# Kernel optimization log

Measured on AMD Instinct MI355X. Metric: run time of the kernel, lower is better.

The kernel has to match this reference:

```python
import jax, jax.numpy as jnp
import numpy as np

N = 100_000   # nodes
D = 64        # hidden = H * C
H, C = 8, 8   # heads, per-head channels
E = 500_000   # edges per edge set
EPS = 1e-3    # keras LayerNormalization default epsilon
RSQRT_C = np.float32(1.0 / np.sqrt(C))


def setup_inputs() -> dict:
    key = jax.random.key(0)
    ks = jax.random.split(key, 13)
    s = 0.05
    return dict(
        x=jax.random.normal(ks[0], (N, D), jnp.float32),
        src0=jax.random.randint(ks[1], (E,), 0, N, jnp.int32),
        dst0=jax.random.randint(ks[2], (E,), 0, N, jnp.int32),
        src1=jax.random.randint(ks[3], (E,), 0, N, jnp.int32),
        dst1=jax.random.randint(ks[4], (E,), 0, N, jnp.int32),
        Wk=jax.random.normal(ks[5], (D, D), jnp.float32) * s,
        bk=jnp.zeros((D,), jnp.float32),
        Wm=jax.random.normal(ks[6], (D, D), jnp.float32) * s,
        bm=jnp.zeros((D,), jnp.float32),
        Wq=jax.random.normal(ks[7], (D, D), jnp.float32) * s,
        bq=jnp.zeros((D,), jnp.float32),
        Wa=jax.random.normal(ks[8], (D, D), jnp.float32) * s,
        ba=jnp.zeros((D,), jnp.float32),
        Watt0=jax.random.normal(ks[9], (H, C, C), jnp.float32) * s,
        Wmsg0=jax.random.normal(ks[10], (H, C, C), jnp.float32) * s,
        prior0=jnp.ones((H,), jnp.float32),
        Watt1=jax.random.normal(ks[11], (H, C, C), jnp.float32) * s,
        Wmsg1=jax.random.normal(ks[12], (H, C, C), jnp.float32) * s,
        prior1=jnp.ones((H,), jnp.float32),
        skip_w=jnp.ones((1,), jnp.float32),
        ln_gamma=jnp.ones((D,), jnp.float32),
        ln_beta=jnp.zeros((D,), jnp.float32),
    )


def _edge_terms(k, m, q, src, dst, Watt, Wmsg, prior):
    # gather sender keys/messages, apply per-edge-set per-head projections
    ke = jnp.einsum('ehk,hkl->ehl', k[src], Watt)          # [E,H,C]
    score = jnp.einsum('ehc,ehc->eh', ke, q[dst]) * prior * RSQRT_C  # [E,H]
    me = jnp.einsum('ehk,hkl->ehl', m[src], Wmsg)          # [E,H,C]
    return score, me


def _forward(x, src0, dst0, src1, dst1, Wk, bk, Wm, bm, Wq, bq, Wa, ba,
             Watt0, Wmsg0, prior0, Watt1, Wmsg1, prior1,
             skip_w, ln_gamma, ln_beta):
    n = x.shape[0]
    split = lambda t: t.reshape(n, H, C)
    k = split(x @ Wk + bk)   # sender keys   [N,H,C]
    m = split(x @ Wm + bm)   # sender msgs   [N,H,C]
    q = split(x @ Wq + bq)   # receiver qrys [N,H,C]

    s0, m0 = _edge_terms(k, m, q, src0, dst0, Watt0, Wmsg0, prior0)
    s1, m1 = _edge_terms(k, m, q, src1, dst1, Watt1, Wmsg1, prior1)

    # joint segment softmax over ALL incoming edges per receiver (across edge sets)
    scores = jnp.concatenate([s0, s1], axis=0)  # [Et,H]
    msgs = jnp.concatenate([m0, m1], axis=0)    # [Et,H,C]
    recv = jnp.concatenate([dst0, dst1], axis=0)
    smax = jax.ops.segment_max(scores, recv, num_segments=n)
    ex = jnp.exp(scores - smax[recv])
    denom = jax.ops.segment_sum(ex, recv, num_segments=n)
    coef = ex / denom[recv]                      # [Et,H]

    pooled = jax.ops.segment_sum(coef[:, :, None] * msgs, recv, num_segments=n)  # [N,H,C]
    merged = pooled.reshape(n, D)
    agg = jax.nn.gelu(merged, approximate=False) @ Wa + ba
    # (dropout_rate=0.0 -> identity)
    sc = jax.nn.sigmoid(skip_w[0])               # learnable weighted skip
    out = sc * agg + (1.0 - sc) * x
    # layer norm (keras default eps=1e-3)
    mu = jnp.mean(out, axis=-1, keepdims=True)
    var = jnp.var(out, axis=-1, keepdims=True)
    return ln_gamma * (out - mu) * jax.lax.rsqrt(var + EPS) + ln_beta


def reference(x, src0, dst0, src1, dst1, Wk, bk, Wm, bm, Wq, bq, Wa, ba,
              Watt0, Wmsg0, prior0, Watt1, Wmsg1, prior1,
              skip_w, ln_gamma, ln_beta):
    return _forward(x, src0, dst0, src1, dst1, Wk, bk, Wm, bm, Wq, bq, Wa, ba,
                    Watt0, Wmsg0, prior0, Watt1, Wmsg1, prior1,
                    skip_w, ln_gamma, ln_beta)
```

## Files before the change

### kernel.cpp

```cpp
#include <hip/hip_runtime.h>
#include <cstdint>
#include <cstddef>

#define TPB 256
static constexpr float RSQRT_C_F = 0.35355339059327373f;

typedef __attribute__((ext_vector_type(8))) short bf16x8;
typedef __attribute__((ext_vector_type(4))) float f32x4;

__device__ __forceinline__ unsigned short f2bf(float f) {
    unsigned u = __float_as_uint(f);
    u += 0x7FFFu + ((u >> 16) & 1u);
    return (unsigned short)(u >> 16);
}
__device__ __forceinline__ float bf2f(unsigned short h) {
    return __uint_as_float((unsigned)h << 16);
}

__global__ void prep1_kernel(const float* __restrict__ Wq, const float* __restrict__ bq,
                             const float* __restrict__ Wk, const float* __restrict__ bk,
                             const float* __restrict__ Wm, const float* __restrict__ bm,
                             const float* __restrict__ Watt0, const float* __restrict__ prior0,
                             const float* __restrict__ Watt1, const float* __restrict__ prior1,
                             const float* __restrict__ Wmsg0, const float* __restrict__ Wmsg1,
                             float* __restrict__ Wbig, float* __restrict__ bbig) {
    int idx = blockIdx.x * TPB + threadIdx.x;
    if (idx < 64 * 320) {
        int i = idx / 320, col = idx % 320;
        float v;
        if (col < 64) {
            v = Wq[i * 64 + col];
        } else {
            int j = col - 64, set = j >> 6, l = j & 63, h = l >> 3, lc = l & 7;
            const float* Win = (set < 2) ? Wk : Wm;
            const float* T = (set == 0) ? Watt0 : (set == 1) ? Watt1 : (set == 2) ? Wmsg0 : Wmsg1;
            float scale = (set == 0) ? prior0[h] * RSQRT_C_F
                        : (set == 1) ? prior1[h] * RSQRT_C_F : 1.f;
            float acc = 0.f;
            #pragma unroll
            for (int c = 0; c < 8; c++) acc += Win[i * 64 + h * 8 + c] * T[h * 64 + c * 8 + lc];
            v = acc * scale;
        }
        Wbig[idx] = v;
    } else if (idx < 64 * 320 + 320) {
        int col = idx - 64 * 320;
        float v;
        if (col < 64) {
            v = bq[col];
        } else {
            int j = col - 64, set = j >> 6, l = j & 63, h = l >> 3, lc = l & 7;
            const float* bin = (set < 2) ? bk : bm;
            const float* T = (set == 0) ? Watt0 : (set == 1) ? Watt1 : (set == 2) ? Wmsg0 : Wmsg1;
            float scale = (set == 0) ? prior0[h] * RSQRT_C_F
                        : (set == 1) ? prior1[h] * RSQRT_C_F : 1.f;
            float acc = 0.f;
            #pragma unroll
            for (int c = 0; c < 8; c++) acc += bin[h * 8 + c] * T[h * 64 + c * 8 + lc];
            v = acc * scale;
        }
        bbig[col] = v;
    }
}

__global__ void prep2_kernel(const float* __restrict__ Wbig, const float* __restrict__ Wa,
                             unsigned short* __restrict__ Wpack,
                             unsigned short* __restrict__ Wapack) {
    int p = blockIdx.x * TPB + threadIdx.x;
    bool isWa = (p >= 40 * 64);
    if (p >= 48 * 64) return;
    int pl = isWa ? p - 40 * 64 : p;
    int lane = pl & 63, ctkt = pl >> 6;
    int ct = ctkt >> 1, kt = ctkt & 1;
    int kbase = kt * 32 + (lane >> 4) * 8;
    int col = ct * 16 + (lane & 15);
    const float* W = isWa ? Wa : Wbig;
    const int stride = isWa ? 64 : 320;
    unsigned short h[8];
    #pragma unroll
    for (int j = 0; j < 8; j++) h[j] = f2bf(W[(size_t)(kbase + j) * stride + col]);
    uint4 pk;
    pk.x = (unsigned)h[0] | ((unsigned)h[1] << 16);
    pk.y = (unsigned)h[2] | ((unsigned)h[3] << 16);
    pk.z = (unsigned)h[4] | ((unsigned)h[5] << 16);
    pk.w = (unsigned)h[6] | ((unsigned)h[7] << 16);
    unsigned short* dst = isWa ? Wapack : Wpack;
    *(uint4*)&dst[(size_t)pl * 8] = pk;
}

__global__ void hist_kernel(const int* __restrict__ dst0, const int* __restrict__ dst1,
                            int* __restrict__ sub, int* __restrict__ rank,
                            int E0, int Etot, int N) {
    int e = blockIdx.x * TPB + threadIdx.x;
    if (e >= Etot) return;
    int d = (e < E0) ? dst0[e] : dst1[e - E0];
    d = min(max(d, 0), N - 1);
    int s = blockIdx.x & 7;
    rank[e] = atomicAdd(&sub[s * N + d], 1);
}

__global__ void sumsub_kernel(int* __restrict__ sub, int* __restrict__ count, int N) {
    int d = blockIdx.x * TPB + threadIdx.x;
    if (d >= N) return;
    int s = 0;
    #pragma unroll
    for (int b = 0; b < 8; b++) {
        int t = sub[b * N + d];
        sub[b * N + d] = s;
        s += t;
    }
    count[d] = s;
}

__global__ void scan1(const int* __restrict__ count, int* __restrict__ offsets,
                      int* __restrict__ blocksums, int n) {
    __shared__ int sums[TPB];
    int b = blockIdx.x, t = threadIdx.x;
    int base = b * 1024 + t * 4;
    int c0 = (base + 0 < n) ? count[base + 0] : 0;
    int c1 = (base + 1 < n) ? count[base + 1] : 0;
    int c2 = (base + 2 < n) ? count[base + 2] : 0;
    int c3 = (base + 3 < n) ? count[base + 3] : 0;
    int local = c0 + c1 + c2 + c3;
    sums[t] = local;
    __syncthreads();
    for (int off = 1; off < TPB; off <<= 1) {
        int add = (t >= off) ? sums[t - off] : 0;
        __syncthreads();
        sums[t] += add;
        __syncthreads();
    }
    int excl = sums[t] - local;
    if (base + 0 < n) offsets[base + 0] = excl;
    if (base + 1 < n) offsets[base + 1] = excl + c0;
    if (base + 2 < n) offsets[base + 2] = excl + c0 + c1;
    if (base + 3 < n) offsets[base + 3] = excl + c0 + c1 + c2;
    if (t == TPB - 1) blocksums[b] = sums[TPB - 1];
}

__global__ void scan2(int* __restrict__ blocksums, int nb) {
    __shared__ int s[TPB];
    int t = threadIdx.x;
    int v = (t < nb) ? blocksums[t] : 0;
    s[t] = v;
    __syncthreads();
    for (int off = 1; off < TPB; off <<= 1) {
        int add = (t >= off) ? s[t - off] : 0;
        __syncthreads();
        s[t] += add;
        __syncthreads();
    }
    if (t < nb) blocksums[t] = s[t] - v;
}

__global__ void scan3(int* __restrict__ offsets, const int* __restrict__ blocksums,
                      int* __restrict__ sub, int n, int Etot) {
    int i = blockIdx.x * TPB + threadIdx.x;
    if (i < n) {
        int v = offsets[i] + blocksums[i >> 10];
        offsets[i] = v;
        #pragma unroll
        for (int b = 0; b < 8; b++) sub[b * n + i] += v;
    }
    if (i == n) offsets[n] = Etot;
}

__global__ void scatter_kernel(const int* __restrict__ src0, const int* __restrict__ dst0,
                               const int* __restrict__ src1, const int* __restrict__ dst1,
                               const int* __restrict__ sub,
                               const int* __restrict__ rank, unsigned* __restrict__ records,
                               int E0, int Etot, int N) {
    int e = blockIdx.x * TPB + threadIdx.x;
    if (e >= Etot) return;
    int s, d, setbit;
    if (e < E0) { s = src0[e]; d = dst0[e]; setbit = 0; }
    else        { s = src1[e - E0]; d = dst1[e - E0]; setbit = 1; }
    d = min(max(d, 0), N - 1);
    int sb = (e >> 8) & 7;
    int pos = sub[sb * N + d] + rank[e];
    pos = min(max(pos, 0), Etot - 1);
    records[pos] = (unsigned)s | ((unsigned)setbit << 24);
}

__global__ __launch_bounds__(TPB) void proj_mfma(const float* __restrict__ x,
                                                 const unsigned short* __restrict__ Wpack,
                                                 const float* __restrict__ bbig,
                                                 float* __restrict__ qbuf,
                                                 unsigned short* __restrict__ kmbuf,
                                                 int N) {
    const int lane = threadIdx.x & 63;
    const int wv = threadIdx.x >> 6;
    const int rowbase = blockIdx.x * 64 + wv * 16;
    const int arow = min(rowbase + (lane & 15), N - 1);
    const int kbase = (lane >> 4) * 8;

    bf16x8 afrag[2];
    #pragma unroll
    for (int kt = 0; kt < 2; kt++) {
        const float* xp = x + (size_t)arow * 64 + kt * 32 + kbase;
        float4 v0 = *(const float4*)xp;
        float4 v1 = *(const float4*)(xp + 4);
        bf16x8 a;
        a[0] = (short)f2bf(v0.x); a[1] = (short)f2bf(v0.y);
        a[2] = (short)f2bf(v0.z); a[3] = (short)f2bf(v0.w);
        a[4] = (short)f2bf(v1.x); a[5] = (short)f2bf(v1.y);
        a[6] = (short)f2bf(v1.z); a[7] = (short)f2bf(v1.w);
        afrag[kt] = a;
    }

    const int colq = lane & 15;
    const int rgrp = (lane >> 4) * 4;

    for (int ct = 0; ct < 20; ct++) {
        bf16x8 b0 = *(const bf16x8*)(Wpack + ((size_t)(ct * 2 + 0) * 64 + lane) * 8);
        bf16x8 b1 = *(const bf16x8*)(Wpack + ((size_t)(ct * 2 + 1) * 64 + lane) * 8);
        f32x4 acc = {0.f, 0.f, 0.f, 0.f};
        acc = __builtin_amdgcn_mfma_f32_16x16x32_bf16(afrag[0], b0, acc, 0, 0, 0);
        acc = __builtin_amdgcn_mfma_f32_16x16x32_bf16(afrag[1], b1, acc, 0, 0, 0);
        const int col = ct * 16 + colq;
        const float bv = bbig[col];
        if (ct < 4) {
            #pragma unroll
            for (int r = 0; r < 4; r++) {
                int row = rowbase + rgrp + r;
                if (row < N) qbuf[(size_t)row * 64 + col] = acc[r] + bv;
            }
        } else {
            const int kmcol = col - 64;
            #pragma unroll
            for (int r = 0; r < 4; r++) {
                int row = rowbase + rgrp + r;
                if (row < N) kmbuf[(size_t)row * 256 + kmcol] = f2bf(acc[r] + bv);
            }
        }
    }
}

__global__ __launch_bounds__(TPB) void pool_kernel(const float* __restrict__ qbuf,
                                                   const unsigned short* __restrict__ kmbuf,
                                                   const unsigned* __restrict__ records,
                                                   const int* __restrict__ offsets,
                                                   float* __restrict__ pooledN,
                                                   int N, int Etot) {
    const int lane = threadIdx.x & 63;
    const int wid = (blockIdx.x * TPB + threadIdx.x) >> 6;
    if (wid >= N) return;
    int beg = offsets[wid], end = offsets[wid + 1];
    beg = min(max(beg, 0), Etot);
    end = min(max(end, beg), Etot);

    const int e_idx = lane >> 3;
    const int j = lane & 7;
    const float NEG_INF = __int_as_float(0xff800000);

    const float* qp = qbuf + (size_t)wid * 64 + (j << 3);
    float4 q0 = *(const float4*)qp;
    float4 q1 = *(const float4*)(qp + 4);

    float m_run = NEG_INF, d_run = 0.f;
    float p0 = 0.f, p1 = 0.f, p2 = 0.f, p3 = 0.f, p4 = 0.f, p5 = 0.f, p6 = 0.f, p7 = 0.f;

    for (int cb = beg; cb < end; cb += 8) {
        int n8 = end - cb;
        if (n8 > 8) n8 = 8;
        unsigned rec = records[cb + min(e_idx, n8 - 1)];
        int sn = min((int)(rec & 0xFFFFFFu), N - 1);
        int st = (rec >> 24) & 1;
        const unsigned short* base = kmbuf + ((size_t)sn << 8) + (st << 6) + (j << 3);
        uint4 kv = *(const uint4*)base;
        uint4 mv = *(const uint4*)(base + 128);

        float s = __uint_as_float(kv.x << 16)         * q0.x
                + __uint_as_float(kv.x & 0xffff0000u) * q0.y
                + __uint_as_float(kv.y << 16)         * q0.z
                + __uint_as_float(kv.y & 0xffff0000u) * q0.w
                + __uint_as_float(kv.z << 16)         * q1.x
                + __uint_as_float(kv.z & 0xffff0000u) * q1.y
                + __uint_as_float(kv.w << 16)         * q1.z
                + __uint_as_float(kv.w & 0xffff0000u) * q1.w;
        if (e_idx >= n8) s = NEG_INF;

        float cm = s;
        cm = fmaxf(cm, __shfl_xor(cm, 8, 64));
        cm = fmaxf(cm, __shfl_xor(cm, 16, 64));
        cm = fmaxf(cm, __shfl_xor(cm, 32, 64));

        if (!__all(cm <= m_run + 8.0f)) {
            float mN = fmaxf(m_run, cm);
            float al = __expf(m_run - mN);
            d_run *= al;
            p0 *= al; p1 *= al; p2 *= al; p3 *= al;
            p4 *= al; p5 *= al; p6 *= al; p7 *= al;
            m_run = mN;
        }

        float coef = __expf(s - m_run);
        d_run += coef;
        p0 += coef * __uint_as_float(mv.x << 16);
        p1 += coef * __uint_as_float(mv.x & 0xffff0000u);
        p2 += coef * __uint_as_float(mv.y << 16);
        p3 += coef * __uint_as_float(mv.y & 0xffff0000u);
        p4 += coef * __uint_as_float(mv.z << 16);
        p5 += coef * __uint_as_float(mv.z & 0xffff0000u);
        p6 += coef * __uint_as_float(mv.w << 16);
        p7 += coef * __uint_as_float(mv.w & 0xffff0000u);
    }

#define XRED(v) v += __shfl_xor(v, 8, 64); v += __shfl_xor(v, 16, 64); v += __shfl_xor(v, 32, 64)
    XRED(p0); XRED(p1); XRED(p2); XRED(p3);
    XRED(p4); XRED(p5); XRED(p6); XRED(p7);
    XRED(d_run);
#undef XRED

    float v = p0;
    v = (e_idx == 1) ? p1 : v;
    v = (e_idx == 2) ? p2 : v;
    v = (e_idx == 3) ? p3 : v;
    v = (e_idx == 4) ? p4 : v;
    v = (e_idx == 5) ? p5 : v;
    v = (e_idx == 6) ? p6 : v;
    v = (e_idx == 7) ? p7 : v;
    const int ch = (j << 3) | e_idx;
    pooledN[(size_t)wid * 64 + ch] = (end > beg) ? v / d_run : 0.f;
}

__global__ __launch_bounds__(TPB) void final_mfma(const float* __restrict__ x,
                                                  const float* __restrict__ pooledN,
                                                  const unsigned short* __restrict__ Wapack,
                                                  const float* __restrict__ ba,
                                                  const float* __restrict__ skipw,
                                                  const float* __restrict__ gamma,
                                                  const float* __restrict__ beta,
                                                  float* __restrict__ out, int N) {
    const int lane = threadIdx.x & 63;
    const int wv = threadIdx.x >> 6;
    const int rowbase = blockIdx.x * 64 + wv * 16;
    const int arow = min(rowbase + (lane & 15), N - 1);
    const int kbase = (lane >> 4) * 8;
    const float sc = 1.f / (1.f + __expf(-skipw[0]));

    bf16x8 afrag[2];
    #pragma unroll
    for (int kt = 0; kt < 2; kt++) {
        const float* pp = pooledN + (size_t)arow * 64 + kt * 32 + kbase;
        float4 v0 = *(const float4*)pp;
        float4 v1 = *(const float4*)(pp + 4);
        float g[8] = {v0.x, v0.y, v0.z, v0.w, v1.x, v1.y, v1.z, v1.w};
        bf16x8 a;
        #pragma unroll
        for (int i = 0; i < 8; i++) {
            float gg = 0.5f * g[i] * (1.f + erff(g[i] * 0.70710678118654752f));
            a[i] = (short)f2bf(gg);
        }
        afrag[kt] = a;
    }

    const int colq = lane & 15;
    const int rgrp = (lane >> 4) * 4;

    float o[4][4];
    #pragma unroll
    for (int ct = 0; ct < 4; ct++) {
        bf16x8 b0 = *(const bf16x8*)(Wapack + ((size_t)(ct * 2 + 0) * 64 + lane) * 8);
        bf16x8 b1 = *(const bf16x8*)(Wapack + ((size_t)(ct * 2 + 1) * 64 + lane) * 8);
        f32x4 acc = {0.f, 0.f, 0.f, 0.f};
        acc = __builtin_amdgcn_mfma_f32_16x16x32_bf16(afrag[0], b0, acc, 0, 0, 0);
        acc = __builtin_amdgcn_mfma_f32_16x16x32_bf16(afrag[1], b1, acc, 0, 0, 0);
        const int col = ct * 16 + colq;
        const float bav = ba[col];
        #pragma unroll
        for (int r = 0; r < 4; r++) {
            int row = min(rowbase + rgrp + r, N - 1);
            float xv = x[(size_t)row * 64 + col];
            o[ct][r] = sc * (acc[r] + bav) + (1.f - sc) * xv;
        }
    }

    #pragma unroll
    for (int r = 0; r < 4; r++) {
        float s1 = o[0][r] + o[1][r] + o[2][r] + o[3][r];
        float s2 = o[0][r] * o[0][r] + o[1][r] * o[1][r]
                 + o[2][r] * o[2][r] + o[3][r] * o[3][r];
        #pragma unroll
        for (int off = 1; off <= 8; off <<= 1) {
            s1 += __shfl_xor(s1, off, 64);
            s2 += __shfl_xor(s2, off, 64);
        }
        float mu = s1 * (1.f / 64.f);
        float var = s2 * (1.f / 64.f) - mu * mu;
        float rs = rsqrtf(var + 1e-3f);
        const int row = rowbase + rgrp + r;
        if (row < N) {
            #pragma unroll
            for (int ct = 0; ct < 4; ct++) {
                const int col = ct * 16 + colq;
                out[(size_t)row * 64 + col] = gamma[col] * (o[ct][r] - mu) * rs + beta[col];
            }
        }
    }
}

extern "C" void kernel_launch(void* const* d_in, const int* in_sizes, int n_in,
                              void* d_out, int out_size, void* d_ws, size_t ws_size,
                              hipStream_t stream) {
    const float* x      = (const float*)d_in[0];
    const int*   src0   = (const int*)d_in[1];
    const int*   dst0   = (const int*)d_in[2];
    const int*   src1   = (const int*)d_in[3];
    const int*   dst1   = (const int*)d_in[4];
    const float* Wk     = (const float*)d_in[5];
    const float* bk     = (const float*)d_in[6];
    const float* Wm     = (const float*)d_in[7];
    const float* bm     = (const float*)d_in[8];
    const float* Wq     = (const float*)d_in[9];
    const float* bq     = (const float*)d_in[10];
    const float* Wa     = (const float*)d_in[11];
    const float* ba     = (const float*)d_in[12];
    const float* Watt0  = (const float*)d_in[13];
    const float* Wmsg0  = (const float*)d_in[14];
    const float* prior0 = (const float*)d_in[15];
    const float* Watt1  = (const float*)d_in[16];
    const float* Wmsg1  = (const float*)d_in[17];
    const float* prior1 = (const float*)d_in[18];
    const float* skipw  = (const float*)d_in[19];
    const float* gamma  = (const float*)d_in[20];
    const float* beta   = (const float*)d_in[21];

    const int N  = in_sizes[0] / 64;
    const int E0 = in_sizes[1];
    const int E1 = in_sizes[3];
    const int Etot = E0 + E1;

    float* ws       = (float*)d_ws;
    float* Wbig     = ws;
    float* bbig     = Wbig + 64 * 320;
    unsigned short* Wpack  = (unsigned short*)(bbig + 320);
    unsigned short* Wapack = Wpack + 40 * 64 * 8;
    float* qbuf     = (float*)(Wapack + 8 * 64 * 8);
    float* pooledN  = qbuf + (size_t)N * 64;
    unsigned short* kmbuf = (unsigned short*)(pooledN + (size_t)N * 64);
    int* sub        = (int*)(kmbuf + (size_t)N * 256);
    int* count      = sub + (size_t)8 * N;
    int* offsets    = count + N;
    int* blocksums  = offsets + N + 1;
    int* rank       = blocksums + 512;
    unsigned* records = (unsigned*)(rank + Etot);

    const int nb1 = (N + 1023) / 1024;
    const int gE = (Etot + TPB - 1) / TPB;

    prep1_kernel<<<(64 * 320 + 320 + TPB - 1) / TPB, TPB, 0, stream>>>(
        Wq, bq, Wk, bk, Wm, bm, Watt0, prior0, Watt1, prior1, Wmsg0, Wmsg1, Wbig, bbig);
    hipMemsetAsync(sub, 0, (size_t)8 * N * sizeof(int), stream);
    prep2_kernel<<<(48 * 64 + TPB - 1) / TPB, TPB, 0, stream>>>(Wbig, Wa, Wpack, Wapack);

    proj_mfma<<<(N + 63) / 64, TPB, 0, stream>>>(x, Wpack, bbig, qbuf, kmbuf, N);

    hist_kernel<<<gE, TPB, 0, stream>>>(dst0, dst1, sub, rank, E0, Etot, N);
    sumsub_kernel<<<(N + TPB - 1) / TPB, TPB, 0, stream>>>(sub, count, N);

    scan1<<<nb1, TPB, 0, stream>>>(count, offsets, blocksums, N);
    scan2<<<1, TPB, 0, stream>>>(blocksums, nb1);
    scan3<<<(N + 1 + TPB - 1) / TPB, TPB, 0, stream>>>(offsets, blocksums, sub, N, Etot);

    scatter_kernel<<<gE, TPB, 0, stream>>>(src0, dst0, src1, dst1, sub,
                                           rank, records, E0, Etot, N);

    pool_kernel<<<(N * 64 + TPB - 1) / TPB, TPB, 0, stream>>>(qbuf, kmbuf, records, offsets,
                                                              pooledN, N, Etot);

    final_mfma<<<(N + 63) / 64, TPB, 0, stream>>>(x, pooledN, Wapack, ba, skipw,
                                                  gamma, beta, (float*)d_out, N);
}
```

Measured before the change: 169.4 us.

## Store q and pooled buffers in bf16 and process two edge chunks per iteration

The query buffer and the pooled-output buffer are now stored as bf16 instead of fp32, which halves their write and read traffic between the projection, pooling and final kernels. The pooling loop also handles 16 edges per iteration as two 8-edge chunks, issuing both gathers before the online-softmax update. This adds memory-level parallelism and halves the number of max-reduction shuffles. It trades extra precision loss in q and the pooled values, plus higher register pressure in the pool kernel.

```diff
diff --git a/kernel.cpp b/kernel.cpp
--- a/kernel.cpp
+++ b/kernel.cpp
@@ -15,6 +15,16 @@
 }
 __device__ __forceinline__ float bf2f(unsigned short h) {
     return __uint_as_float((unsigned)h << 16);
+}
+__device__ __forceinline__ float dot8bf(uint4 k, const float* qa) {
+    return __uint_as_float(k.x << 16)         * qa[0]
+         + __uint_as_float(k.x & 0xffff0000u) * qa[1]
+         + __uint_as_float(k.y << 16)         * qa[2]
+         + __uint_as_float(k.y & 0xffff0000u) * qa[3]
+         + __uint_as_float(k.z << 16)         * qa[4]
+         + __uint_as_float(k.z & 0xffff0000u) * qa[5]
+         + __uint_as_float(k.w << 16)         * qa[6]
+         + __uint_as_float(k.w & 0xffff0000u) * qa[7];
 }
 
 __global__ void prep1_kernel(const float* __restrict__ Wq, const float* __restrict__ bq,
@@ -184,7 +194,7 @@
 __global__ __launch_bounds__(TPB) void proj_mfma(const float* __restrict__ x,
                                                  const unsigned short* __restrict__ Wpack,
                                                  const float* __restrict__ bbig,
-                                                 float* __restrict__ qbuf,
+                                                 unsigned short* __restrict__ qbuf,
                                                  unsigned short* __restrict__ kmbuf,
                                                  int N) {
     const int lane = threadIdx.x & 63;
@@ -222,7 +232,7 @@
             #pragma unroll
             for (int r = 0; r < 4; r++) {
                 int row = rowbase + rgrp + r;
-                if (row < N) qbuf[(size_t)row * 64 + col] = acc[r] + bv;
+                if (row < N) qbuf[(size_t)row * 64 + col] = f2bf(acc[r] + bv);
             }
         } else {
             const int kmcol = col - 64;
@@ -235,11 +245,11 @@
     }
 }
 
-__global__ __launch_bounds__(TPB) void pool_kernel(const float* __restrict__ qbuf,
+__global__ __launch_bounds__(TPB) void pool_kernel(const unsigned short* __restrict__ qbuf,
                                                    const unsigned short* __restrict__ kmbuf,
                                                    const unsigned* __restrict__ records,
                                                    const int* __restrict__ offsets,
-                                                   float* __restrict__ pooledN,
+                                                   unsigned short* __restrict__ pooledN,
                                                    int N, int Etot) {
     const int lane = threadIdx.x & 63;
     const int wid = (blockIdx.x * TPB + threadIdx.x) >> 6;
@@ -252,34 +262,38 @@
     const int j = lane & 7;
     const float NEG_INF = __int_as_float(0xff800000);
 
-    const float* qp = qbuf + (size_t)wid * 64 + (j << 3);
-    float4 q0 = *(const float4*)qp;
-    float4 q1 = *(const float4*)(qp + 4);
+    uint4 qv = *(const uint4*)(qbuf + (size_t)wid * 64 + (j << 3));
+    float qa[8];
+    qa[0] = __uint_as_float(qv.x << 16); qa[1] = __uint_as_float(qv.x & 0xffff0000u);
+    qa[2] = __uint_as_float(qv.y << 16); qa[3] = __uint_as_float(qv.y & 0xffff0000u);
+    qa[4] = __uint_as_float(qv.z << 16); qa[5] = __uint_as_float(qv.z & 0xffff0000u);
+    qa[6] = __uint_as_float(qv.w << 16); qa[7] = __uint_as_float(qv.w & 0xffff0000u);
 
     float m_run = NEG_INF, d_run = 0.f;
     float p0 = 0.f, p1 = 0.f, p2 = 0.f, p3 = 0.f, p4 = 0.f, p5 = 0.f, p6 = 0.f, p7 = 0.f;
 
-    for (int cb = beg; cb < end; cb += 8) {
-        int n8 = end - cb;
-        if (n8 > 8) n8 = 8;
-        unsigned rec = records[cb + min(e_idx, n8 - 1)];
-        int sn = min((int)(rec & 0xFFFFFFu), N - 1);
-        int st = (rec >> 24) & 1;
-        const unsigned short* base = kmbuf + ((size_t)sn << 8) + (st << 6) + (j << 3);
-        uint4 kv = *(const uint4*)base;
-        uint4 mv = *(const uint4*)(base + 128);
-
-        float s = __uint_as_float(kv.x << 16)         * q0.x
-                + __uint_as_float(kv.x & 0xffff0000u) * q0.y
-                + __uint_as_float(kv.y << 16)         * q0.z
-                + __uint_as_float(kv.y & 0xffff0000u) * q0.w
-                + __uint_as_float(kv.z << 16)         * q1.x
-                + __uint_as_float(kv.z & 0xffff0000u) * q1.y
-                + __uint_as_float(kv.w << 16)         * q1.z
-                + __uint_as_float(kv.w & 0xffff0000u) * q1.w;
-        if (e_idx >= n8) s = NEG_INF;
-
-        float cm = s;
+    for (int cb = beg; cb < end; cb += 16) {
+        const int nA = min(end - cb, 8);
+        const int nB = min(end - cb - 8, 8);
+        unsigned recA = records[cb + min(e_idx, nA - 1)];
+        int idxB = (nB > 0) ? (cb + 8 + min(e_idx, nB - 1)) : (cb);
+        unsigned recB = records[idxB];
+
+        int snA = min((int)(recA & 0xFFFFFFu), N - 1), stA = (recA >> 24) & 1;
+        int snB = min((int)(recB & 0xFFFFFFu), N - 1), stB = (recB >> 24) & 1;
+        const unsigned short* baseA = kmbuf + ((size_t)snA << 8) + (stA << 6) + (j << 3);
+        const unsigned short* baseB = kmbuf + ((size_t)snB << 8) + (stB << 6) + (j << 3);
+        uint4 kA = *(const uint4*)baseA;
+        uint4 mA = *(const uint4*)(baseA + 128);
+        uint4 kB = *(const uint4*)baseB;
+        uint4 mB = *(const uint4*)(baseB + 128);
+
+        float sA = dot8bf(kA, qa);
+        float sB = dot8bf(kB, qa);
+        if (e_idx >= nA) sA = NEG_INF;
+        if (e_idx >= nB) sB = NEG_INF;
+
+        float cm = fmaxf(sA, sB);
         cm = fmaxf(cm, __shfl_xor(cm, 8, 64));
         cm = fmaxf(cm, __shfl_xor(cm, 16, 64));
         cm = fmaxf(cm, __shfl_xor(cm, 32, 64));
@@ -293,16 +307,17 @@
             m_run = mN;
         }
 
-        float coef = __expf(s - m_run);
-        d_run += coef;
-        p0 += coef * __uint_as_float(mv.x << 16);
-        p1 += coef * __uint_as_float(mv.x & 0xffff0000u);
-        p2 += coef * __uint_as_float(mv.y << 16);
-        p3 += coef * __uint_as_float(mv.y & 0xffff0000u);
-        p4 += coef * __uint_as_float(mv.z << 16);
-        p5 += coef * __uint_as_float(mv.z & 0xffff0000u);
-        p6 += coef * __uint_as_float(mv.w << 16);
-        p7 += coef * __uint_as_float(mv.w & 0xffff0000u);
+        float cA = __expf(sA - m_run);
+        float cB = __expf(sB - m_run);
+        d_run += cA + cB;
+        p0 += cA * __uint_as_float(mA.x << 16)         + cB * __uint_as_float(mB.x << 16);
+        p1 += cA * __uint_as_float(mA.x & 0xffff0000u) + cB * __uint_as_float(mB.x & 0xffff0000u);
+        p2 += cA * __uint_as_float(mA.y << 16)         + cB * __uint_as_float(mB.y << 16);
+        p3 += cA * __uint_as_float(mA.y & 0xffff0000u) + cB * __uint_as_float(mB.y & 0xffff0000u);
+        p4 += cA * __uint_as_float(mA.z << 16)         + cB * __uint_as_float(mB.z << 16);
+        p5 += cA * __uint_as_float(mA.z & 0xffff0000u) + cB * __uint_as_float(mB.z & 0xffff0000u);
+        p6 += cA * __uint_as_float(mA.w << 16)         + cB * __uint_as_float(mB.w << 16);
+        p7 += cA * __uint_as_float(mA.w & 0xffff0000u) + cB * __uint_as_float(mB.w & 0xffff0000u);
     }
 
 #define XRED(v) v += __shfl_xor(v, 8, 64); v += __shfl_xor(v, 16, 64); v += __shfl_xor(v, 32, 64)
@@ -320,11 +335,11 @@
     v = (e_idx == 6) ? p6 : v;
     v = (e_idx == 7) ? p7 : v;
     const int ch = (j << 3) | e_idx;
-    pooledN[(size_t)wid * 64 + ch] = (end > beg) ? v / d_run : 0.f;
+    pooledN[(size_t)wid * 64 + ch] = f2bf((end > beg) ? v / d_run : 0.f);
 }
 
 __global__ __launch_bounds__(TPB) void final_mfma(const float* __restrict__ x,
-                                                  const float* __restrict__ pooledN,
+                                                  const unsigned short* __restrict__ pooledN,
                                                   const unsigned short* __restrict__ Wapack,
                                                   const float* __restrict__ ba,
                                                   const float* __restrict__ skipw,
@@ -341,10 +356,12 @@
     bf16x8 afrag[2];
     #pragma unroll
     for (int kt = 0; kt < 2; kt++) {
-        const float* pp = pooledN + (size_t)arow * 64 + kt * 32 + kbase;
-        float4 v0 = *(const float4*)pp;
-        float4 v1 = *(const float4*)(pp + 4);
-        float g[8] = {v0.x, v0.y, v0.z, v0.w, v1.x, v1.y, v1.z, v1.w};
+        uint4 pv = *(const uint4*)(pooledN + (size_t)arow * 64 + kt * 32 + kbase);
+        float g[8];
+        g[0] = __uint_as_float(pv.x << 16); g[1] = __uint_as_float(pv.x & 0xffff0000u);
+        g[2] = __uint_as_float(pv.y << 16); g[3] = __uint_as_float(pv.y & 0xffff0000u);
+        g[4] = __uint_as_float(pv.z << 16); g[5] = __uint_as_float(pv.z & 0xffff0000u);
+        g[6] = __uint_as_float(pv.w << 16); g[7] = __uint_as_float(pv.w & 0xffff0000u);
         bf16x8 a;
         #pragma unroll
         for (int i = 0; i < 8; i++) {
@@ -435,9 +452,9 @@
     float* bbig     = Wbig + 64 * 320;
     unsigned short* Wpack  = (unsigned short*)(bbig + 320);
     unsigned short* Wapack = Wpack + 40 * 64 * 8;
-    float* qbuf     = (float*)(Wapack + 8 * 64 * 8);
-    float* pooledN  = qbuf + (size_t)N * 64;
-    unsigned short* kmbuf = (unsigned short*)(pooledN + (size_t)N * 64);
+    unsigned short* qbuf   = Wapack + 8 * 64 * 8;
+    unsigned short* pooledN = qbuf + (size_t)N * 64;
+    unsigned short* kmbuf  = pooledN + (size_t)N * 64;
     int* sub        = (int*)(kmbuf + (size_t)N * 256);
     int* count      = sub + (size_t)8 * N;
     int* offsets    = count + N;
```

Result: no change. 168.4 us (-0.6%).
